# Performance work log

Measured on AMD Instinct MI355X. Metric: run time of the kernel, lower is better.

Reference implementation:

```python
import jax, jax.numpy as jnp
import numpy as np

N = 100000      # nodes
E = 640000      # edges
V_IN = 128
U_IN = 64
HID = 128
B = 128         # graphs


def setup_inputs() -> dict:
    key = jax.random.key(0)
    ks = jax.random.split(key, 9)
    x = jax.random.normal(ks[0], (N, V_IN), dtype=jnp.float32)
    edge_index = jax.random.randint(ks[1], (2, E), 0, N, dtype=jnp.int64)
    edge_attr = jax.random.normal(ks[2], (E, HID), dtype=jnp.float32)
    u = jax.random.normal(ks[3], (B, U_IN), dtype=jnp.float32)
    batch = jnp.sort(jax.random.randint(ks[4], (N,), 0, B, dtype=jnp.int64))
    fan_in1 = V_IN + HID + U_IN
    W1 = jax.random.normal(ks[5], (fan_in1, HID), dtype=jnp.float32) / np.sqrt(fan_in1)
    b1 = jnp.zeros((HID,), dtype=jnp.float32)
    W2 = jax.random.normal(ks[6], (HID, HID), dtype=jnp.float32) / np.sqrt(HID)
    b2 = jnp.zeros((HID,), dtype=jnp.float32)
    return {"x": x, "edge_index": edge_index, "edge_attr": edge_attr, "u": u,
            "batch": batch, "W1": W1, "b1": b1, "W2": W2, "b2": b2}


def reference(x, edge_index, edge_attr, u, batch, W1, b1, W2, b2):
    col = edge_index[1]
    # scatter_add edge_attr into destination-node slots: [N, HID]
    agg = jax.ops.segment_sum(edge_attr, col, num_segments=x.shape[0])
    # concat [x, agg, u[batch]] -> [N, V_IN + HID + U_IN]
    h = jnp.concatenate([x, agg, u[batch]], axis=1)
    h = jax.nn.relu(h @ W1 + b1)
    return h @ W2 + b2
```

## Files before the change

kernel.cpp:

```cpp
#include <hip/hip_runtime.h>
#include <hip/hip_bf16.h>

#define V_IN 128
#define U_IN 64
#define HID 128
#define K1  (V_IN + HID + U_IN)

typedef __attribute__((ext_vector_type(8))) short bf16x8;
typedef __attribute__((ext_vector_type(4))) float f32x4;

static __device__ __forceinline__ unsigned short f2bf(float f) {
    __hip_bfloat16 h = __float2bfloat16(f);
    union { __hip_bfloat16 h; unsigned short u; } v; v.h = h;
    return v.u;
}
static __device__ __forceinline__ unsigned int f2bf2(float lo, float hi) {
    __hip_bfloat162 h2 = __float22bfloat162_rn(make_float2(lo, hi));
    union { __hip_bfloat162 h; unsigned int u; } v; v.h = h2;
    return v.u;
}

__global__ __launch_bounds__(256) void zero_prep(
    const float* __restrict__ W1, const float* __restrict__ W2,
    unsigned short* __restrict__ Wt1, unsigned short* __restrict__ Wt2,
    int* __restrict__ deg, int N)
{
    int id = blockIdx.x * 256 + threadIdx.x;
    if (id < N) deg[id] = 0;
    if (id < HID * K1) {
        int c = id / K1, k = id - c * K1;
        Wt1[id] = f2bf(W1[(size_t)k * HID + c]);
    }
    if (id < HID * HID) {
        int c = id >> 7, k = id & 127;
        Wt2[id] = f2bf(W2[(size_t)k * HID + c]);
    }
}


__global__ __launch_bounds__(256) void hist_kernel(
    const int* __restrict__ col, int* __restrict__ deg, int E)
{
    int e = blockIdx.x * 256 + threadIdx.x;
    if (e < E) atomicAdd(&deg[col[e]], 1);
}

__global__ __launch_bounds__(256) void scan_partial(
    const int* __restrict__ deg, int* __restrict__ blockSums, int N)
{
    __shared__ int sdata[256];
    int base = blockIdx.x * 1024;
    int tid  = threadIdx.x;
    int s = 0;
    #pragma unroll
    for (int j = 0; j < 4; ++j) {
        int i = base + tid * 4 + j;
        if (i < N) s += deg[i];
    }
    sdata[tid] = s;
    __syncthreads();
    for (int off = 128; off > 0; off >>= 1) {
        if (tid < off) sdata[tid] += sdata[tid + off];
        __syncthreads();
    }
    if (tid == 0) blockSums[blockIdx.x] = sdata[0];
}

__global__ __launch_bounds__(256) void scan_final(
    const int* __restrict__ deg, const int* __restrict__ blockSums,
    int* __restrict__ offsets, int* __restrict__ cur, int N, int E)
{
    __shared__ int sdata[256];
    __shared__ int rdata[256];
    int tid = threadIdx.x;

    int part = 0;
    for (int i = tid; i < (int)blockIdx.x; i += 256) part += blockSums[i];
    rdata[tid] = part;
    __syncthreads();
    for (int off = 128; off > 0; off >>= 1) {
        if (tid < off) rdata[tid] += rdata[tid + off];
        __syncthreads();
    }
    const int blockPrefix = rdata[0];

    int base = blockIdx.x * 1024;
    int loc[4];
    int s = 0;
    #pragma unroll
    for (int j = 0; j < 4; ++j) {
        int i = base + tid * 4 + j;
        loc[j] = (i < N) ? deg[i] : 0;
        s += loc[j];
    }
    int mine = s;
    sdata[tid] = s;
    __syncthreads();
    for (int off = 1; off < 256; off <<= 1) {
        int t = (tid >= off) ? sdata[tid - off] : 0;
        __syncthreads();
        sdata[tid] += t;
        __syncthreads();
    }
    int prefix = blockPrefix + sdata[tid] - mine;
    #pragma unroll
    for (int j = 0; j < 4; ++j) {
        int i = base + tid * 4 + j;
        if (i < N) { offsets[i] = prefix; cur[i] = prefix; prefix += loc[j]; }
    }
    if (blockIdx.x == 0 && tid == 0) offsets[N] = E;
}

__global__ __launch_bounds__(256) void fill_kernel(
    const int* __restrict__ col, int* __restrict__ cur,
    int* __restrict__ eidx, int E)
{
    int e = blockIdx.x * 256 + threadIdx.x;
    if (e < E) {
        int p = atomicAdd(&cur[col[e]], 1);
        eidx[p] = e;
    }
}

#define ROWS 32
#define LDA_E 328
#define LDH_E 136
#define ECAP 1280

__global__ __launch_bounds__(512, 4) void mlp_mfma(
    const float* __restrict__ x,
    const float* __restrict__ edge_attr,
    const int*   __restrict__ offsets,
    const int*   __restrict__ eidx,
    const float* __restrict__ u,
    const int*   __restrict__ batch,
    const unsigned short* __restrict__ Wt1,
    const unsigned short* __restrict__ Wt2,
    const float* __restrict__ b1, const float* __restrict__ b2,
    float* __restrict__ out, int N)
{
    __shared__ __align__(16) unsigned short A[ROWS * LDA_E];
    __shared__ __align__(16) unsigned short H[ROWS * LDH_E];
    __shared__ int Eidx[ECAP];
    const int tid  = threadIdx.x;
    const int n0   = blockIdx.x * ROWS;
    const int lane = tid & 63;
    const int wave = tid >> 6;
    const int l15  = lane & 15;
    const int lhi  = lane >> 4;
    const int wcol = wave * 16 + l15;

    const int nEnd   = (n0 + ROWS < N) ? n0 + ROWS : N;
    const int s_base = offsets[n0];
    const int s_end  = offsets[nEnd];
    const int cnt    = (s_end - s_base < ECAP) ? s_end - s_base : ECAP;
    for (int i = tid; i < cnt; i += 512) Eidx[i] = eidx[s_base + i];

    #pragma unroll
    for (int it = 0; it < 3; ++it) {
        int t   = tid + it * 512;
        int row = t / 48;
        int s   = t - row * 48;
        int n   = n0 + row;
        unsigned short* Arow = &A[row * LDA_E];
        f32x4 v = {0.f, 0.f, 0.f, 0.f};
        int colbase;
        if (s < 32) {
            if (n < N) v = __builtin_nontemporal_load((const f32x4*)(x + (size_t)n * V_IN) + s);
            colbase = s * 4;
        } else {
            if (n < N) {
                int b = batch[n];
                v = *((const f32x4*)(u + (size_t)b * U_IN) + (s - 32));
            }
            colbase = V_IN + HID + (s - 32) * 4;
        }
        uint2 o; o.x = f2bf2(v[0], v[1]); o.y = f2bf2(v[2], v[3]);
        *(uint2*)&Arow[colbase] = o;
    }
    __syncthreads();

    #pragma unroll
    for (int it = 0; it < 2; ++it) {
        int t   = tid + it * 512;
        int row = t >> 5;
        int c   = t & 31;
        int n   = n0 + row;
        f32x4 a0 = {0.f, 0.f, 0.f, 0.f};
        f32x4 a1 = {0.f, 0.f, 0.f, 0.f};
        f32x4 a2 = {0.f, 0.f, 0.f, 0.f};
        f32x4 a3 = {0.f, 0.f, 0.f, 0.f};
        if (n < N) {
            int ls = offsets[n]     - s_base;
            int le = offsets[n + 1] - s_base;
            int j = ls;
            for (; j + 7 < le; j += 8) {
                int e0, e1, e2, e3, e4, e5, e6, e7;
                if (j + 7 < ECAP) {
                    e0 = Eidx[j];     e1 = Eidx[j + 1];
                    e2 = Eidx[j + 2]; e3 = Eidx[j + 3];
                    e4 = Eidx[j + 4]; e5 = Eidx[j + 5];
                    e6 = Eidx[j + 6]; e7 = Eidx[j + 7];
                } else {
                    e0 = eidx[s_base + j];     e1 = eidx[s_base + j + 1];
                    e2 = eidx[s_base + j + 2]; e3 = eidx[s_base + j + 3];
                    e4 = eidx[s_base + j + 4]; e5 = eidx[s_base + j + 5];
                    e6 = eidx[s_base + j + 6]; e7 = eidx[s_base + j + 7];
                }
                f32x4 v0 = __builtin_nontemporal_load((const f32x4*)(edge_attr + (size_t)e0 * HID) + c);
                f32x4 v1 = __builtin_nontemporal_load((const f32x4*)(edge_attr + (size_t)e1 * HID) + c);
                f32x4 v2 = __builtin_nontemporal_load((const f32x4*)(edge_attr + (size_t)e2 * HID) + c);
                f32x4 v3 = __builtin_nontemporal_load((const f32x4*)(edge_attr + (size_t)e3 * HID) + c);
                f32x4 v4 = __builtin_nontemporal_load((const f32x4*)(edge_attr + (size_t)e4 * HID) + c);
                f32x4 v5 = __builtin_nontemporal_load((const f32x4*)(edge_attr + (size_t)e5 * HID) + c);
                f32x4 v6 = __builtin_nontemporal_load((const f32x4*)(edge_attr + (size_t)e6 * HID) + c);
                f32x4 v7 = __builtin_nontemporal_load((const f32x4*)(edge_attr + (size_t)e7 * HID) + c);
                a0 += v0; a1 += v1; a2 += v2; a3 += v3;
                a0 += v4; a1 += v5; a2 += v6; a3 += v7;
            }
            if (j + 3 < le) {
                int e0, e1, e2, e3;
                if (j + 3 < ECAP) {
                    e0 = Eidx[j];     e1 = Eidx[j + 1];
                    e2 = Eidx[j + 2]; e3 = Eidx[j + 3];
                } else {
                    e0 = eidx[s_base + j];     e1 = eidx[s_base + j + 1];
                    e2 = eidx[s_base + j + 2]; e3 = eidx[s_base + j + 3];
                }
                f32x4 v0 = __builtin_nontemporal_load((const f32x4*)(edge_attr + (size_t)e0 * HID) + c);
                f32x4 v1 = __builtin_nontemporal_load((const f32x4*)(edge_attr + (size_t)e1 * HID) + c);
                f32x4 v2 = __builtin_nontemporal_load((const f32x4*)(edge_attr + (size_t)e2 * HID) + c);
                f32x4 v3 = __builtin_nontemporal_load((const f32x4*)(edge_attr + (size_t)e3 * HID) + c);
                a0 += v0; a1 += v1; a2 += v2; a3 += v3;
                j += 4;
            }
            for (; j < le; ++j) {
                int e0 = (j < ECAP) ? Eidx[j] : eidx[s_base + j];
                a0 += __builtin_nontemporal_load((const f32x4*)(edge_attr + (size_t)e0 * HID) + c);
            }
        }
        f32x4 asum = (a0 + a1) + (a2 + a3);
        uint2 o;
        o.x = f2bf2(asum[0], asum[1]);
        o.y = f2bf2(asum[2], asum[3]);
        *(uint2*)&A[row * LDA_E + V_IN + c * 4] = o;
    }

    __builtin_amdgcn_sched_barrier(0);

    bf16x8 w1f[10], w2f[4];
    #pragma unroll
    for (int ks = 0; ks < 10; ++ks)
        w1f[ks] = *(const bf16x8*)(Wt1 + (size_t)wcol * K1 + ks * 32 + lhi * 8);
    #pragma unroll
    for (int ks = 0; ks < 4; ++ks)
        w2f[ks] = *(const bf16x8*)(Wt2 + (size_t)wcol * HID + ks * 32 + lhi * 8);
    const float b1v = b1[wcol];
    const float b2v = b2[wcol];

    __syncthreads();

    f32x4 acc[2] = {{0.f, 0.f, 0.f, 0.f}, {0.f, 0.f, 0.f, 0.f}};
    #pragma unroll
    for (int ks = 0; ks < 10; ++ks) {
        #pragma unroll
        for (int h = 0; h < 2; ++h) {
            bf16x8 af = *(const bf16x8*)&A[(h * 16 + l15) * LDA_E + ks * 32 + lhi * 8];
            acc[h] = __builtin_amdgcn_mfma_f32_16x16x32_bf16(af, w1f[ks], acc[h], 0, 0, 0);
        }
    }
    #pragma unroll
    for (int h = 0; h < 2; ++h)
        #pragma unroll
        for (int r = 0; r < 4; ++r) {
            float hv = fmaxf(acc[h][r] + b1v, 0.f);
            H[(h * 16 + lhi * 4 + r) * LDH_E + wcol] = f2bf(hv);
        }
    __syncthreads();

    f32x4 acc2[2] = {{0.f, 0.f, 0.f, 0.f}, {0.f, 0.f, 0.f, 0.f}};
    #pragma unroll
    for (int ks = 0; ks < 4; ++ks) {
        #pragma unroll
        for (int h = 0; h < 2; ++h) {
            bf16x8 hf = *(const bf16x8*)&H[(h * 16 + l15) * LDH_E + ks * 32 + lhi * 8];
            acc2[h] = __builtin_amdgcn_mfma_f32_16x16x32_bf16(hf, w2f[ks], acc2[h], 0, 0, 0);
        }
    }
    #pragma unroll
    for (int h = 0; h < 2; ++h)
        #pragma unroll
        for (int r = 0; r < 4; ++r) {
            int n = n0 + h * 16 + lhi * 4 + r;
            if (n < N)
                __builtin_nontemporal_store(acc2[h][r] + b2v, out + (size_t)n * HID + wcol);
        }
}

extern "C" void kernel_launch(void* const* d_in, const int* in_sizes, int n_in,
                              void* d_out, int out_size, void* d_ws, size_t ws_size,
                              hipStream_t stream) {
    const float* x          = (const float*)d_in[0];
    const int*   edge_index = (const int*)  d_in[1];
    const float* edge_attr  = (const float*)d_in[2];
    const float* u          = (const float*)d_in[3];
    const int*   batch      = (const int*)  d_in[4];
    const float* W1         = (const float*)d_in[5];
    const float* b1         = (const float*)d_in[6];
    const float* W2         = (const float*)d_in[7];
    const float* b2         = (const float*)d_in[8];
    float* out = (float*)d_out;

    const int N = in_sizes[0] / V_IN;
    const int E = in_sizes[1] / 2;
    const int* col = edge_index + E;

    unsigned short* Wt1  = (unsigned short*)d_ws;
    unsigned short* Wt2  = Wt1 + (size_t)K1 * HID;
    int* deg       = (int*)(Wt2 + (size_t)HID * HID);
    int* cur       = deg + N;
    int* offsets   = cur + N;
    int* blockSums = offsets + N + 1;
    int* eidx      = blockSums + 2048;

    const int NB = (N + 1023) / 1024;
    const int ZP = ((N > HID * K1 ? N : HID * K1) + 255) / 256;

    zero_prep   <<<ZP, 256, 0, stream>>>(W1, W2, Wt1, Wt2, deg, N);
    hist_kernel <<<(E + 255) / 256, 256, 0, stream>>>(col, deg, E);
    scan_partial<<<NB, 256, 0, stream>>>(deg, blockSums, N);
    scan_final  <<<NB, 256, 0, stream>>>(deg, blockSums, offsets, cur, N, E);
    fill_kernel <<<(E + 255) / 256, 256, 0, stream>>>(col, cur, eidx, E);

    mlp_mfma<<<(N + ROWS - 1) / ROWS, 512, 0, stream>>>(
        x, edge_attr, offsets, eidx, u, batch, Wt1, Wt2, b1, b2, out, N);
}
```

Baseline: 216.1 us.

## Stage CSR offsets in LDS, shrink gather unroll, drop nontemporal hints and sched barrier

Loads the block's CSR offsets into shared memory once so each row reads its edge range from LDS instead of global memory. The edge gather loop is cut from 8-wide plus a 4-wide tail to a plain 4-wide loop, which lowers register pressure but keeps fewer loads in flight. Nontemporal hints are removed from the x loads and the output stores, and the scheduling barrier before the weight-fragment loads is dropped. This lets the compiler overlap those weight loads with the gather, at the cost of less explicit control over instruction order.

```diff
diff --git a/kernel.cpp b/kernel.cpp
--- a/kernel.cpp
+++ b/kernel.cpp
@@ -142,6 +142,7 @@
     __shared__ __align__(16) unsigned short A[ROWS * LDA_E];
     __shared__ __align__(16) unsigned short H[ROWS * LDH_E];
     __shared__ int Eidx[ECAP];
+    __shared__ int Soff[ROWS + 1];
     const int tid  = threadIdx.x;
     const int n0   = blockIdx.x * ROWS;
     const int lane = tid & 63;
@@ -151,6 +152,10 @@
     const int wcol = wave * 16 + l15;
 
     const int nEnd   = (n0 + ROWS < N) ? n0 + ROWS : N;
+    if (tid <= ROWS) {
+        int idx = n0 + tid;
+        Soff[tid] = offsets[(idx < nEnd) ? idx : nEnd];
+    }
     const int s_base = offsets[n0];
     const int s_end  = offsets[nEnd];
     const int cnt    = (s_end - s_base < ECAP) ? s_end - s_base : ECAP;
@@ -163,19 +168,19 @@
         int s   = t - row * 48;
         int n   = n0 + row;
         unsigned short* Arow = &A[row * LDA_E];
-        f32x4 v = {0.f, 0.f, 0.f, 0.f};
+        float4 v = make_float4(0.f, 0.f, 0.f, 0.f);
         int colbase;
         if (s < 32) {
-            if (n < N) v = __builtin_nontemporal_load((const f32x4*)(x + (size_t)n * V_IN) + s);
+            if (n < N) v = ((const float4*)(x + (size_t)n * V_IN))[s];
             colbase = s * 4;
         } else {
             if (n < N) {
                 int b = batch[n];
-                v = *((const f32x4*)(u + (size_t)b * U_IN) + (s - 32));
+                v = ((const float4*)(u + (size_t)b * U_IN))[s - 32];
             }
             colbase = V_IN + HID + (s - 32) * 4;
         }
-        uint2 o; o.x = f2bf2(v[0], v[1]); o.y = f2bf2(v[2], v[3]);
+        uint2 o; o.x = f2bf2(v.x, v.y); o.y = f2bf2(v.z, v.w);
         *(uint2*)&Arow[colbase] = o;
     }
     __syncthreads();
@@ -191,34 +196,10 @@
         f32x4 a2 = {0.f, 0.f, 0.f, 0.f};
         f32x4 a3 = {0.f, 0.f, 0.f, 0.f};
         if (n < N) {
-            int ls = offsets[n]     - s_base;
-            int le = offsets[n + 1] - s_base;
+            int ls = Soff[row]     - s_base;
+            int le = Soff[row + 1] - s_base;
             int j = ls;
-            for (; j + 7 < le; j += 8) {
-                int e0, e1, e2, e3, e4, e5, e6, e7;
-                if (j + 7 < ECAP) {
-                    e0 = Eidx[j];     e1 = Eidx[j + 1];
-                    e2 = Eidx[j + 2]; e3 = Eidx[j + 3];
-                    e4 = Eidx[j + 4]; e5 = Eidx[j + 5];
-                    e6 = Eidx[j + 6]; e7 = Eidx[j + 7];
-                } else {
-                    e0 = eidx[s_base + j];     e1 = eidx[s_base + j + 1];
-                    e2 = eidx[s_base + j + 2]; e3 = eidx[s_base + j + 3];
-                    e4 = eidx[s_base + j + 4]; e5 = eidx[s_base + j + 5];
-                    e6 = eidx[s_base + j + 6]; e7 = eidx[s_base + j + 7];
-                }
-                f32x4 v0 = __builtin_nontemporal_load((const f32x4*)(edge_attr + (size_t)e0 * HID) + c);
-                f32x4 v1 = __builtin_nontemporal_load((const f32x4*)(edge_attr + (size_t)e1 * HID) + c);
-                f32x4 v2 = __builtin_nontemporal_load((const f32x4*)(edge_attr + (size_t)e2 * HID) + c);
-                f32x4 v3 = __builtin_nontemporal_load((const f32x4*)(edge_attr + (size_t)e3 * HID) + c);
-                f32x4 v4 = __builtin_nontemporal_load((const f32x4*)(edge_attr + (size_t)e4 * HID) + c);
-                f32x4 v5 = __builtin_nontemporal_load((const f32x4*)(edge_attr + (size_t)e5 * HID) + c);
-                f32x4 v6 = __builtin_nontemporal_load((const f32x4*)(edge_attr + (size_t)e6 * HID) + c);
-                f32x4 v7 = __builtin_nontemporal_load((const f32x4*)(edge_attr + (size_t)e7 * HID) + c);
-                a0 += v0; a1 += v1; a2 += v2; a3 += v3;
-                a0 += v4; a1 += v5; a2 += v6; a3 += v7;
-            }
-            if (j + 3 < le) {
+            for (; j + 3 < le; j += 4) {
                 int e0, e1, e2, e3;
                 if (j + 3 < ECAP) {
                     e0 = Eidx[j];     e1 = Eidx[j + 1];
@@ -232,7 +213,6 @@
                 f32x4 v2 = __builtin_nontemporal_load((const f32x4*)(edge_attr + (size_t)e2 * HID) + c);
                 f32x4 v3 = __builtin_nontemporal_load((const f32x4*)(edge_attr + (size_t)e3 * HID) + c);
                 a0 += v0; a1 += v1; a2 += v2; a3 += v3;
-                j += 4;
             }
             for (; j < le; ++j) {
                 int e0 = (j < ECAP) ? Eidx[j] : eidx[s_base + j];
@@ -246,8 +226,6 @@
         *(uint2*)&A[row * LDA_E + V_IN + c * 4] = o;
     }
 
-    __builtin_amdgcn_sched_barrier(0);
-
     bf16x8 w1f[10], w2f[4];
     #pragma unroll
     for (int ks = 0; ks < 10; ++ks)
@@ -292,8 +270,7 @@
         #pragma unroll
         for (int r = 0; r < 4; ++r) {
             int n = n0 + h * 16 + lhi * 4 + r;
-            if (n < N)
-                __builtin_nontemporal_store(acc2[h][r] + b2v, out + (size_t)n * HID + wcol);
+            if (n < N) out[(size_t)n * HID + wcol] = acc2[h][r] + b2v;
         }
 }
 
```

New measurement: 201.5 us. 6.8% less time.
